# Kernel tuning notes

Measured on AMD Instinct MI355X. Metric: run time of the kernel, lower is better.

Reference implementation:

```python
import jax, jax.numpy as jnp
import numpy as np

H = 16          # bit depth
N_K = 2         # random masks per flipped bit
TP = 8          # location dims per node
CUR_TP = 4      # dims updated per step
CUR_PORTION = 0.8
N = 1 << H      # location value range
T = 1024        # stations
S = 64          # neighbors per station
D = 256         # embedding dim
C = 2 * H * N_K + 1  # candidate locations per station


def _cos_sim(a, b):
    # frexp-based integer 'cosine' similarity from CritiGraph.cos_similarity
    sg = jnp.where(a >= 0, 1.0, -1.0) * jnp.where(b >= 0, 1.0, -1.0)
    x = ((jnp.abs(a) ^ jnp.abs(b)) + 1).astype(jnp.float32)
    _, e = jnp.frexp(x)  # exponent = bit length of (xor+1)
    return sg * (1.0 - e.astype(jnp.float32) / H)


def _connection(ori, rand_numbers):
    # ori: [T,tp] int64, rand_numbers: [T,H,N_K,tp] int64 in [0, N)
    bits = jnp.int64(1) << jnp.arange(H, dtype=jnp.int64)          # [H]
    flipped = ori[:, None, :] ^ bits[None, :, None]                # [T,H,tp]
    masks = rand_numbers & (bits - 1)[None, :, None, None]        # low-k-bit masks
    res = (flipped[:, :, None, :] ^ masks).reshape(ori.shape[0], H * N_K, TP)
    # candidate order: flipped variants, original (index H*N_K ... wait: res has H*N_K), original, negated
    return jnp.concatenate([res, ori[:, None, :], -res], axis=1)  # [T,C,tp]


def setup_inputs() -> dict:
    key = jax.random.key(0)
    ks = jax.random.split(key, 8)
    return {
        "sta_loc": jax.random.randint(ks[0], (T, TP), 1 - N, N, dtype=jnp.int64),
        "nei_loc": jax.random.randint(ks[1], (T, S, TP), 1 - N, N, dtype=jnp.int64),
        "rand_numbers": jax.random.randint(ks[2], (T, H, N_K, TP), 0, N, dtype=jnp.int64),
        "sta_emb": jax.random.normal(ks[3], (T, D), dtype=jnp.float32),
        "nei_emb": jax.random.normal(ks[4], (T, S, D), dtype=jnp.float32),
        "mask": (jax.random.uniform(ks[5], (T, S)) > 0.1).astype(jnp.float32),
        "rand_vals": jax.random.uniform(ks[6], (T, TP), dtype=jnp.float32),
        "t_rand": jax.random.uniform(ks[7], (T,), dtype=jnp.float32),
    }


def _forward(sta_loc, nei_loc, rand_numbers, sta_emb, nei_emb, mask, rand_vals, t_rand):
    cnc_loc = _connection(sta_loc, rand_numbers)                    # [T,C,tp]
    # euclidean-space cosine targets
    sta_n = sta_emb / jnp.linalg.norm(sta_emb, axis=-1, keepdims=True)
    nei_n = nei_emb / jnp.linalg.norm(nei_emb, axis=-1, keepdims=True)
    eu_val = jnp.einsum("td,tsd->ts", sta_n, nei_n)                 # [T,S]
    # ct_val swap-one-dim kernel (= ct_val_triton math)
    cos_sn = _cos_sim(sta_loc[:, None, :], nei_loc)                 # [T,S,tp]
    cos_sn_sum = cos_sn.sum(axis=-1)                                # [T,S]
    cos_cn = _cos_sim(cnc_loc[:, None, :, :], nei_loc[:, :, None, :])  # [T,S,C,tp]
    ct_val = (cos_sn_sum[:, :, None, None] - cos_sn[:, :, None, :] + cos_cn) / TP
    # masked squared cosine loss (loom_valid)
    lth = mask.sum(axis=1) + 1e-12                                  # [T]
    eu = eu_val[:, :, None, None]
    loss = jnp.square(ct_val - eu) * jnp.abs(eu) * mask[:, :, None, None]
    loss = loss.sum(axis=1) / lth[:, None, None]                    # [T,C,tp]
    # get_best_loc argmin routing
    argmin_all = jnp.argmin(loss, axis=1)                           # [T,tp]
    base = jnp.full((T, TP), H * N_K, dtype=argmin_all.dtype)       # index of original loc
    rand_cols = jnp.argsort(rand_vals, axis=1)[:, :CUR_TP]          # [T,cur_tp]
    sel = t_rand < CUR_PORTION                                      # [T]
    rows = jnp.broadcast_to(jnp.arange(T)[:, None], (T, CUR_TP))
    upd = jnp.where(sel[:, None], argmin_all[rows, rand_cols], base[rows, rand_cols])
    cnc_idx = base.at[rows, rand_cols].set(upd)                     # [T,tp]
    ti = jnp.arange(T)[:, None]
    di = jnp.arange(TP)[None, :]
    selected_locs = cnc_loc[ti, cnc_idx, di]                        # [T,tp]
    real_loss = loss[ti, cnc_idx, di].mean(axis=-1)                 # [T]
    return selected_locs, real_loss


def reference(sta_loc, nei_loc, rand_numbers, sta_emb, nei_emb, mask, rand_vals, t_rand):
    return _forward(sta_loc, nei_loc, rand_numbers, sta_emb, nei_emb, mask, rand_vals, t_rand)
```

## Files before the change

kernel.cpp:

```cpp
#include <hip/hip_runtime.h>
#include <math.h>

#define T_  1024
#define S_  64
#define D_  256
#define TP_ 8
#define C_  65

__device__ __forceinline__ int cnc_val(int c, int sl, const int* rn_row, int p) {
    if (c == 32) return sl;
    int cc = (c < 32) ? c : (c - 33);
    int h = cc >> 1, k = cc & 1;
    int m = rn_row[h * 16 + k * 8 + p] & ((1 << h) - 1);
    int v = (sl ^ (1 << h)) ^ m;
    return (c < 32) ? v : -v;
}

__device__ __forceinline__ float cos_sim_i(int a, int b) {
    float sg = ((a >= 0) == (b >= 0)) ? 1.0f : -1.0f;
    int aa = a < 0 ? -a : a;
    int bb = b < 0 ? -b : b;
    int x = (aa ^ bb) + 1;
    int e = 32 - __clz(x);
    return sg * (1.0f - (float)e * 0.0625f);
}

__global__ __launch_bounds__(256, 4) void critigraph_kernel(
    const int* __restrict__ sta_loc,
    const int* __restrict__ nei_loc,
    const int* __restrict__ rand_numbers,
    const float* __restrict__ sta_emb,
    const float* __restrict__ nei_emb,
    const float* __restrict__ mask,
    const float* __restrict__ rand_vals,
    const float* __restrict__ t_rand,
    float* __restrict__ out_sel,
    float* __restrict__ out_loss)
{
    const int t = blockIdx.x;
    const int tid = threadIdx.x;
    const int lane = tid & 63;
    const int wave = tid >> 6;

    __shared__ __align__(16) float s_sta[D_];
    __shared__ __align__(16) float4 s_cb[512];
    __shared__ int   s_nl[512];
    __shared__ int   s_rn[256];
    __shared__ int   s_sl[8];
    __shared__ float s_m[64];
    __shared__ float s_rv[8];
    __shared__ float s_cs[512];
    __shared__ float s_css[64];
    __shared__ float s_eun[64];
    __shared__ float s_eu[64];
    __shared__ float s_w[64];
    __shared__ float s_loss[C_ * 8];
    __shared__ float s_red[4];
    __shared__ float s_inv, s_lth;
    __shared__ int   s_amin[8];
    __shared__ int   s_cidx[8];

    const int srow = tid >> 2, j4 = tid & 3;
    const float4* nrow = reinterpret_cast<const float4*>(nei_emb + (size_t)t * S_ * D_);
    float4 nv[16];
#pragma unroll
    for (int i = 0; i < 16; i++) nv[i] = nrow[srow * 64 + i * 4 + j4];

    float stav = sta_emb[t * D_ + tid];
    s_sta[tid] = stav;
    s_nl[tid]       = nei_loc[t * 512 + tid];
    s_nl[tid + 256] = nei_loc[t * 512 + tid + 256];
    s_rn[tid] = rand_numbers[t * 256 + tid];
    if (tid < 8) { s_sl[tid] = sta_loc[t * 8 + tid]; s_rv[tid] = rand_vals[t * 8 + tid]; }
    if (tid < 64) s_m[tid] = mask[t * 64 + tid];
    __syncthreads();

    {
        s_cs[tid]       = cos_sim_i(s_sl[tid & 7], s_nl[tid]);
        s_cs[tid + 256] = cos_sim_i(s_sl[tid & 7], s_nl[tid + 256]);
        float sq = stav * stav;
#pragma unroll
        for (int off = 32; off; off >>= 1) sq += __shfl_xor(sq, off, 64);
        if (lane == 0) s_red[wave] = sq;
        if (wave == 1) {
            float mv = s_m[lane];
#pragma unroll
            for (int off = 32; off; off >>= 1) mv += __shfl_xor(mv, off, 64);
            if (lane == 0) s_lth = mv + 1e-12f;
        }
    }
    __syncthreads();

    if (tid == 0) s_inv = 1.0f / sqrtf(s_red[0] + s_red[1] + s_red[2] + s_red[3]);
    if (tid < 64) {
        float a = s_cs[tid * 8];
        for (int p = 1; p < 8; p++) a += s_cs[tid * 8 + p];
        s_css[tid] = a;
    }
    {
        const float4* st4 = reinterpret_cast<const float4*>(s_sta);
        float d0 = 0.f, n0 = 0.f;
#pragma unroll
        for (int i = 0; i < 16; i++) {
            float4 sv = st4[i * 4 + j4];
            float4 nn = nv[i];
            d0 = fmaf(nn.x, sv.x, d0); d0 = fmaf(nn.y, sv.y, d0);
            d0 = fmaf(nn.z, sv.z, d0); d0 = fmaf(nn.w, sv.w, d0);
            n0 = fmaf(nn.x, nn.x, n0); n0 = fmaf(nn.y, nn.y, n0);
            n0 = fmaf(nn.z, nn.z, n0); n0 = fmaf(nn.w, nn.w, n0);
        }
        d0 += __shfl_xor(d0, 1, 64); d0 += __shfl_xor(d0, 2, 64);
        n0 += __shfl_xor(n0, 1, 64); n0 += __shfl_xor(n0, 2, 64);
        if (j4 == 0) s_eun[srow] = d0 * (1.0f / sqrtf(n0));
    }
    __syncthreads();

#pragma unroll
    for (int q = tid; q < 512; q += 256) {
        int s = q >> 3;
        int nl = s_nl[q];
        int code = (nl < 0) ? (int)(0x80000000u | (unsigned)(-nl)) : nl;
        float g = s_css[s] - s_cs[q];
        float eu = s_eun[s] * s_inv;
        float w = fabsf(eu) * s_m[s];
        s_cb[q] = make_float4(__int_as_float(code), g, eu, w);
        if ((q & 7) == 0) { s_eu[s] = eu; s_w[s] = w; }
    }
    __syncthreads();

    {
        const float lth = s_lth;
        const int c = tid >> 3, p = tid & 7;
        int v = cnc_val(c, s_sl[p], s_rn, p);
        unsigned avc  = (v < 0) ? (0x80000000u | (unsigned)(-v)) : (unsigned)v;
        unsigned flip = (v != 0) ? 0x80000000u : 0u;
        float acc1 = 0.f, acc2 = 0.f;
#pragma unroll 4
        for (int s = 0; s < 64; s++) {
            float4 cb = s_cb[s * 8 + p];
            unsigned y = avc ^ (unsigned)__float_as_int(cb.x);
            int x = (int)(y & 0x7fffffffu) + 1;
            float ccu = fmaf((float)__clz(x), 0.0625f, -1.0f);
            unsigned ccb = __float_as_uint(ccu) ^ (y & 0x80000000u);
            float cc1 = __uint_as_float(ccb);
            float cc2 = __uint_as_float(ccb ^ flip);
            float d1 = fmaf(cb.y + cc1, 0.125f, -cb.z);
            float d2 = fmaf(cb.y + cc2, 0.125f, -cb.z);
            acc1 = fmaf(d1 * d1, cb.w, acc1);
            acc2 = fmaf(d2 * d2, cb.w, acc2);
        }
        s_loss[c * 8 + p]        = acc1 / lth;
        s_loss[(c + 33) * 8 + p] = acc2 / lth;
        if (tid < 8) {
            float a32 = 0.f;
            for (int s = 0; s < 64; s++) {
                float d = fmaf(s_css[s], 0.125f, -s_eu[s]);
                a32 = fmaf(d * d, s_w[s], a32);
            }
            s_loss[256 + tid] = a32 / lth;
        }
    }
    __syncthreads();

    if (tid < 64) {
        const int p = tid >> 3, g = tid & 7;
        float bv = s_loss[g * 8 + p];
        int bi = g;
        for (int k = 1; k < 8; k++) {
            int c = g + 8 * k;
            float vv = s_loss[c * 8 + p];
            if (vv < bv) { bv = vv; bi = c; }
        }
        if (g == 0) {
            float vv = s_loss[512 + p];
            if (vv < bv) { bv = vv; bi = 64; }
        }
#pragma unroll
        for (int off = 1; off < 8; off <<= 1) {
            float ov = __shfl_xor(bv, off, 64);
            int   oi = __shfl_xor(bi, off, 64);
            if (ov < bv || (ov == bv && oi < bi)) { bv = ov; bi = oi; }
        }
        if (g == 0) s_amin[p] = bi;
    }
    __syncthreads();

    if (tid == 0) {
        bool sel = t_rand[t] < 0.8f;
        float rv[8]; int cidx[8]; bool taken[8];
        for (int p = 0; p < 8; p++) { rv[p] = s_rv[p]; cidx[p] = 32; taken[p] = false; }
        for (int j = 0; j < 4; j++) {
            int bi = -1; float bvv = 0.f;
            for (int p = 0; p < 8; p++) {
                if (taken[p]) continue;
                if (bi < 0 || rv[p] < bvv) { bi = p; bvv = rv[p]; }
            }
            taken[bi] = true;
            cidx[bi] = sel ? s_amin[bi] : 32;
        }
        for (int p = 0; p < 8; p++) s_cidx[p] = cidx[p];
    }
    __syncthreads();

    if (tid < 8) {
        int c = s_cidx[tid];
        out_sel[t * 8 + tid] = (float)cnc_val(c, s_sl[tid], s_rn, tid);
    }
    if (tid == 64) {
        float a = 0.f;
        for (int p = 0; p < 8; p++) a += s_loss[s_cidx[p] * 8 + p];
        out_loss[t] = a * 0.125f;
    }
}

extern "C" void kernel_launch(void* const* d_in, const int* in_sizes, int n_in,
                              void* d_out, int out_size, void* d_ws, size_t ws_size,
                              hipStream_t stream) {
    const int*   sta_loc      = (const int*)d_in[0];
    const int*   nei_loc      = (const int*)d_in[1];
    const int*   rand_numbers = (const int*)d_in[2];
    const float* sta_emb      = (const float*)d_in[3];
    const float* nei_emb      = (const float*)d_in[4];
    const float* mask         = (const float*)d_in[5];
    const float* rand_vals    = (const float*)d_in[6];
    const float* t_rand       = (const float*)d_in[7];

    float* out_sel  = (float*)d_out;
    float* out_loss = out_sel + T_ * TP_;

    critigraph_kernel<<<T_, 256, 0, stream>>>(
        sta_loc, nei_loc, rand_numbers, sta_emb, nei_emb, mask,
        rand_vals, t_rand, out_sel, out_loss);
}
```

Before: 113.4 us.

## Cut block barriers by merging stages and replacing serial selection with parallel rank

Restructures the per-station kernel so it needs fewer __syncthreads. The station norm is folded into the neighbour dot-product loop, the cosine-sum precompute is computed per row in registers, and the serial single-thread top-4 selection is replaced by a parallel rank computation with shuffles. All global loads, including t_rand, are issued up front, and the shared buffers shrink from a float4 record to float2 pairs. The risk is some redundant per-thread work, since each thread recomputes 8 cosines per row, plus a slightly different reduction order for the norm.

```diff
diff --git a/kernel.cpp b/kernel.cpp
--- a/kernel.cpp
+++ b/kernel.cpp
@@ -1,28 +1,26 @@
 #include <hip/hip_runtime.h>
 #include <math.h>
 
-#define T_  1024
-#define S_  64
-#define D_  256
-#define TP_ 8
-#define C_  65
-
-__device__ __forceinline__ int cnc_val(int c, int sl, const int* rn_row, int p) {
+#define T_ 1024
+
+__device__ __forceinline__ unsigned icode(int v) {
+    return (v < 0) ? (0x80000000u | (unsigned)(-v)) : (unsigned)v;
+}
+
+__device__ __forceinline__ float cosc(unsigned ca, unsigned cb) {
+    unsigned y = ca ^ cb;
+    int x = (int)(y & 0x7fffffffu) + 1;
+    float m = fmaf((float)__clz(x), 0.0625f, -1.0f);
+    return __uint_as_float(__float_as_uint(m) ^ (y & 0x80000000u));
+}
+
+__device__ __forceinline__ int cnc_val(int c, int sl, const int* rn, int p) {
     if (c == 32) return sl;
     int cc = (c < 32) ? c : (c - 33);
     int h = cc >> 1, k = cc & 1;
-    int m = rn_row[h * 16 + k * 8 + p] & ((1 << h) - 1);
+    int m = rn[h * 16 + k * 8 + p] & ((1 << h) - 1);
     int v = (sl ^ (1 << h)) ^ m;
     return (c < 32) ? v : -v;
-}
-
-__device__ __forceinline__ float cos_sim_i(int a, int b) {
-    float sg = ((a >= 0) == (b >= 0)) ? 1.0f : -1.0f;
-    int aa = a < 0 ? -a : a;
-    int bb = b < 0 ? -b : b;
-    int x = (aa ^ bb) + 1;
-    int e = 32 - __clz(x);
-    return sg * (1.0f - (float)e * 0.0625f);
 }
 
 __global__ __launch_bounds__(256, 4) void critigraph_kernel(
@@ -39,67 +37,73 @@
 {
     const int t = blockIdx.x;
     const int tid = threadIdx.x;
-    const int lane = tid & 63;
-    const int wave = tid >> 6;
-
-    __shared__ __align__(16) float s_sta[D_];
-    __shared__ __align__(16) float4 s_cb[512];
-    __shared__ int   s_nl[512];
-    __shared__ int   s_rn[256];
-    __shared__ int   s_sl[8];
-    __shared__ float s_m[64];
-    __shared__ float s_rv[8];
-    __shared__ float s_cs[512];
-    __shared__ float s_css[64];
-    __shared__ float s_eun[64];
-    __shared__ float s_eu[64];
-    __shared__ float s_w[64];
-    __shared__ float s_loss[C_ * 8];
-    __shared__ float s_red[4];
-    __shared__ float s_inv, s_lth;
-    __shared__ int   s_amin[8];
-    __shared__ int   s_cidx[8];
-
     const int srow = tid >> 2, j4 = tid & 3;
-    const float4* nrow = reinterpret_cast<const float4*>(nei_emb + (size_t)t * S_ * D_);
+    const int c = tid >> 3, p = tid & 7;
+
+    __shared__ __align__(16) float    s_sta[256];
+    __shared__ __align__(16) unsigned s_nlc[512];
+    __shared__ __align__(16) int      s_rn[256];
+    __shared__ __align__(8)  float2   s_cg[512];
+    __shared__ __align__(8)  float2   s_ew[64];
+    __shared__ float  s_css[64];
+    __shared__ float  s_loss[520];
+    __shared__ int    s_sl[8];
+    __shared__ unsigned s_slc[8];
+    __shared__ float  s_m[64];
+    __shared__ float  s_rv[8];
+    __shared__ float  s_lth;
+
+    float stav = sta_emb[t * 256 + tid];
+    int nl0 = nei_loc[t * 512 + tid];
+    int nl1 = nei_loc[t * 512 + 256 + tid];
+    int rnv = rand_numbers[t * 256 + tid];
+    int slv = 0; float rvv = 0.f;
+    if (tid < 8) { slv = sta_loc[t * 8 + tid]; rvv = rand_vals[t * 8 + tid]; }
+    float mv = (tid < 64) ? mask[t * 64 + tid] : 0.f;
+    float trv = t_rand[t];
+
+    const float4* nrow = reinterpret_cast<const float4*>(nei_emb + (size_t)t * 64 * 256);
     float4 nv[16];
 #pragma unroll
     for (int i = 0; i < 16; i++) nv[i] = nrow[srow * 64 + i * 4 + j4];
 
-    float stav = sta_emb[t * D_ + tid];
     s_sta[tid] = stav;
-    s_nl[tid]       = nei_loc[t * 512 + tid];
-    s_nl[tid + 256] = nei_loc[t * 512 + tid + 256];
-    s_rn[tid] = rand_numbers[t * 256 + tid];
-    if (tid < 8) { s_sl[tid] = sta_loc[t * 8 + tid]; s_rv[tid] = rand_vals[t * 8 + tid]; }
-    if (tid < 64) s_m[tid] = mask[t * 64 + tid];
+    s_nlc[tid]       = icode(nl0);
+    s_nlc[tid + 256] = icode(nl1);
+    s_rn[tid] = rnv;
+    if (tid < 8) { s_sl[tid] = slv; s_slc[tid] = icode(slv); s_rv[tid] = rvv; }
+    if (tid < 64) s_m[tid] = mv;
     __syncthreads();
 
+    if ((tid >> 6) == 1) {
+        float x = s_m[tid & 63];
+#pragma unroll
+        for (int off = 32; off; off >>= 1) x += __shfl_xor(x, off, 64);
+        if ((tid & 63) == 0) s_lth = x + 1e-12f;
+    }
+
     {
-        s_cs[tid]       = cos_sim_i(s_sl[tid & 7], s_nl[tid]);
-        s_cs[tid + 256] = cos_sim_i(s_sl[tid & 7], s_nl[tid + 256]);
-        float sq = stav * stav;
-#pragma unroll
-        for (int off = 32; off; off >>= 1) sq += __shfl_xor(sq, off, 64);
-        if (lane == 0) s_red[wave] = sq;
-        if (wave == 1) {
-            float mv = s_m[lane];
-#pragma unroll
-            for (int off = 32; off; off >>= 1) mv += __shfl_xor(mv, off, 64);
-            if (lane == 0) s_lth = mv + 1e-12f;
-        }
-    }
-    __syncthreads();
-
-    if (tid == 0) s_inv = 1.0f / sqrtf(s_red[0] + s_red[1] + s_red[2] + s_red[3]);
-    if (tid < 64) {
-        float a = s_cs[tid * 8];
-        for (int p = 1; p < 8; p++) a += s_cs[tid * 8 + p];
-        s_css[tid] = a;
-    }
+        unsigned slc[8];
+#pragma unroll
+        for (int i = 0; i < 8; i++) slc[i] = s_slc[i];
+        const uint4* nl4 = reinterpret_cast<const uint4*>(s_nlc);
+        const int s0 = tid >> 3;
+#pragma unroll
+        for (int half = 0; half < 2; half++) {
+            int s = s0 + half * 32;
+            uint4 ra = nl4[s * 2], rb = nl4[s * 2 + 1];
+            unsigned nn[8] = {ra.x, ra.y, ra.z, ra.w, rb.x, rb.y, rb.z, rb.w};
+            float css = 0.f, csm[8];
+#pragma unroll
+            for (int i = 0; i < 8; i++) { csm[i] = cosc(slc[i], nn[i]); css += csm[i]; }
+            if (p == 0) s_css[s] = css;
+            s_cg[s * 8 + p] = make_float2(__uint_as_float(nn[p]), css - csm[p]);
+        }
+    }
+
     {
         const float4* st4 = reinterpret_cast<const float4*>(s_sta);
-        float d0 = 0.f, n0 = 0.f;
+        float d0 = 0.f, n0 = 0.f, a0 = 0.f;
 #pragma unroll
         for (int i = 0; i < 16; i++) {
             float4 sv = st4[i * 4 + j4];
@@ -108,54 +112,51 @@
             d0 = fmaf(nn.z, sv.z, d0); d0 = fmaf(nn.w, sv.w, d0);
             n0 = fmaf(nn.x, nn.x, n0); n0 = fmaf(nn.y, nn.y, n0);
             n0 = fmaf(nn.z, nn.z, n0); n0 = fmaf(nn.w, nn.w, n0);
+            a0 = fmaf(sv.x, sv.x, a0); a0 = fmaf(sv.y, sv.y, a0);
+            a0 = fmaf(sv.z, sv.z, a0); a0 = fmaf(sv.w, sv.w, a0);
         }
         d0 += __shfl_xor(d0, 1, 64); d0 += __shfl_xor(d0, 2, 64);
         n0 += __shfl_xor(n0, 1, 64); n0 += __shfl_xor(n0, 2, 64);
-        if (j4 == 0) s_eun[srow] = d0 * (1.0f / sqrtf(n0));
-    }
+        a0 += __shfl_xor(a0, 1, 64); a0 += __shfl_xor(a0, 2, 64);
+        if (j4 == 0) {
+            float eun = d0 * (1.0f / sqrtf(n0));
+            float eu  = eun * (1.0f / sqrtf(a0));
+            float w   = fabsf(eu) * s_m[srow];
+            s_ew[srow] = make_float2(eu, w);
+        }
+    }
+
+    int vcn = cnc_val(c, s_sl[p], s_rn, p);
+    unsigned avc  = icode(vcn);
+    unsigned flip = (vcn != 0) ? 0x80000000u : 0u;
     __syncthreads();
 
-#pragma unroll
-    for (int q = tid; q < 512; q += 256) {
-        int s = q >> 3;
-        int nl = s_nl[q];
-        int code = (nl < 0) ? (int)(0x80000000u | (unsigned)(-nl)) : nl;
-        float g = s_css[s] - s_cs[q];
-        float eu = s_eun[s] * s_inv;
-        float w = fabsf(eu) * s_m[s];
-        s_cb[q] = make_float4(__int_as_float(code), g, eu, w);
-        if ((q & 7) == 0) { s_eu[s] = eu; s_w[s] = w; }
-    }
-    __syncthreads();
-
     {
-        const float lth = s_lth;
-        const int c = tid >> 3, p = tid & 7;
-        int v = cnc_val(c, s_sl[p], s_rn, p);
-        unsigned avc  = (v < 0) ? (0x80000000u | (unsigned)(-v)) : (unsigned)v;
-        unsigned flip = (v != 0) ? 0x80000000u : 0u;
         float acc1 = 0.f, acc2 = 0.f;
 #pragma unroll 4
         for (int s = 0; s < 64; s++) {
-            float4 cb = s_cb[s * 8 + p];
-            unsigned y = avc ^ (unsigned)__float_as_int(cb.x);
+            float2 cg = s_cg[s * 8 + p];
+            float2 ew = s_ew[s];
+            unsigned y = avc ^ __float_as_uint(cg.x);
             int x = (int)(y & 0x7fffffffu) + 1;
-            float ccu = fmaf((float)__clz(x), 0.0625f, -1.0f);
-            unsigned ccb = __float_as_uint(ccu) ^ (y & 0x80000000u);
-            float cc1 = __uint_as_float(ccb);
-            float cc2 = __uint_as_float(ccb ^ flip);
-            float d1 = fmaf(cb.y + cc1, 0.125f, -cb.z);
-            float d2 = fmaf(cb.y + cc2, 0.125f, -cb.z);
-            acc1 = fmaf(d1 * d1, cb.w, acc1);
-            acc2 = fmaf(d2 * d2, cb.w, acc2);
-        }
+            float m1 = fmaf((float)__clz(x), 0.0625f, -1.0f);
+            unsigned cb = __float_as_uint(m1) ^ (y & 0x80000000u);
+            float cc1 = __uint_as_float(cb);
+            float cc2 = __uint_as_float(cb ^ flip);
+            float d1 = fmaf(cg.y + cc1, 0.125f, -ew.x);
+            float d2 = fmaf(cg.y + cc2, 0.125f, -ew.x);
+            acc1 = fmaf(d1 * d1, ew.y, acc1);
+            acc2 = fmaf(d2 * d2, ew.y, acc2);
+        }
+        float lth = s_lth;
         s_loss[c * 8 + p]        = acc1 / lth;
         s_loss[(c + 33) * 8 + p] = acc2 / lth;
         if (tid < 8) {
             float a32 = 0.f;
             for (int s = 0; s < 64; s++) {
-                float d = fmaf(s_css[s], 0.125f, -s_eu[s]);
-                a32 = fmaf(d * d, s_w[s], a32);
+                float2 ew = s_ew[s];
+                float d = fmaf(s_css[s], 0.125f, -ew.x);
+                a32 = fmaf(d * d, ew.y, a32);
             }
             s_loss[256 + tid] = a32 / lth;
         }
@@ -163,16 +164,16 @@
     __syncthreads();
 
     if (tid < 64) {
-        const int p = tid >> 3, g = tid & 7;
-        float bv = s_loss[g * 8 + p];
+        const int pp = tid >> 3, g = tid & 7;
+        float bv = s_loss[g * 8 + pp];
         int bi = g;
+#pragma unroll
         for (int k = 1; k < 8; k++) {
-            int c = g + 8 * k;
-            float vv = s_loss[c * 8 + p];
-            if (vv < bv) { bv = vv; bi = c; }
+            float vv = s_loss[(g + 8 * k) * 8 + pp];
+            if (vv < bv) { bv = vv; bi = g + 8 * k; }
         }
         if (g == 0) {
-            float vv = s_loss[512 + p];
+            float vv = s_loss[512 + pp];
             if (vv < bv) { bv = vv; bi = 64; }
         }
 #pragma unroll
@@ -181,35 +182,24 @@
             int   oi = __shfl_xor(bi, off, 64);
             if (ov < bv || (ov == bv && oi < bi)) { bv = ov; bi = oi; }
         }
-        if (g == 0) s_amin[p] = bi;
-    }
-    __syncthreads();
-
-    if (tid == 0) {
-        bool sel = t_rand[t] < 0.8f;
-        float rv[8]; int cidx[8]; bool taken[8];
-        for (int p = 0; p < 8; p++) { rv[p] = s_rv[p]; cidx[p] = 32; taken[p] = false; }
-        for (int j = 0; j < 4; j++) {
-            int bi = -1; float bvv = 0.f;
-            for (int p = 0; p < 8; p++) {
-                if (taken[p]) continue;
-                if (bi < 0 || rv[p] < bvv) { bi = p; bvv = rv[p]; }
-            }
-            taken[bi] = true;
-            cidx[bi] = sel ? s_amin[bi] : 32;
-        }
-        for (int p = 0; p < 8; p++) s_cidx[p] = cidx[p];
-    }
-    __syncthreads();
-
-    if (tid < 8) {
-        int c = s_cidx[tid];
-        out_sel[t * 8 + tid] = (float)cnc_val(c, s_sl[tid], s_rn, tid);
-    }
-    if (tid == 64) {
+        bool sel = trv < 0.8f;
+        float rme = s_rv[pp];
+        int rank = 0;
+#pragma unroll
+        for (int p2 = 0; p2 < 8; p2++) {
+            float ro = s_rv[p2];
+            rank += (ro < rme || (ro == rme && p2 < pp)) ? 1 : 0;
+        }
+        int cidx = (rank < 4 && sel) ? bi : 32;
+        if (g == 0)
+            out_sel[t * 8 + pp] = (float)cnc_val(cidx, s_sl[pp], s_rn, pp);
         float a = 0.f;
-        for (int p = 0; p < 8; p++) a += s_loss[s_cidx[p] * 8 + p];
-        out_loss[t] = a * 0.125f;
+#pragma unroll
+        for (int p2 = 0; p2 < 8; p2++) {
+            int cx = __shfl(cidx, p2 * 8, 64);
+            a += s_loss[cx * 8 + p2];
+        }
+        if (tid == 0) out_loss[t] = a * 0.125f;
     }
 }
 
@@ -226,7 +216,7 @@
     const float* t_rand       = (const float*)d_in[7];
 
     float* out_sel  = (float*)d_out;
-    float* out_loss = out_sel + T_ * TP_;
+    float* out_loss = out_sel + T_ * 8;
 
     critigraph_kernel<<<T_, 256, 0, stream>>>(
         sta_loc, nei_loc, rand_numbers, sta_emb, nei_emb, mask,
```

Measured after the change: 113.0 us. About the same (-0.4%).
